# Kernel tuning notes

Hardware: AMD Instinct MI355X
Metric: run time of the kernel (lower is better)

Reference implementation:

```python
import jax, jax.numpy as jnp
import numpy as np

D_MODEL = 1024
N_HEAD = 16
HEAD_DIM = D_MODEL // N_HEAD
D_INNER = (int(D_MODEL * 2.0) + 7) // 8 * 8  # 2048
EPS = 1e-6


def setup_inputs() -> dict:
    key = jax.random.key(0)
    ks = jax.random.split(key, 8)
    B, T = 2, 2048
    s = 0.02
    return {
        "x": jax.random.normal(ks[0], (B, T, D_MODEL), dtype=jnp.float32),
        "ln1_w": jnp.ones((D_MODEL,), jnp.float32),
        "ln2_w": jnp.ones((D_MODEL,), jnp.float32),
        "qkv_w": jax.random.normal(ks[1], (3 * D_MODEL, D_MODEL), jnp.float32) * s,
        "o_w": jax.random.normal(ks[2], (D_MODEL, D_MODEL), jnp.float32) * s,
        "gate_w": jax.random.normal(ks[3], (D_INNER, D_MODEL), jnp.float32) * s,
        "up_w": jax.random.normal(ks[4], (D_INNER, D_MODEL), jnp.float32) * s,
        "down_w": jax.random.normal(ks[5], (D_MODEL, D_INNER), jnp.float32) * s,
    }


def _rmsnorm(x, w):
    xf = x.astype(jnp.float32)
    rms = jax.lax.rsqrt(jnp.mean(xf * xf, axis=-1, keepdims=True) + EPS)
    return (xf * rms).astype(x.dtype) * w


def _attention(x, qkv_w, o_w):
    B, T, D = x.shape
    qkv = (x @ qkv_w.T).reshape(B, T, 3, N_HEAD, HEAD_DIM)
    q, k, v = qkv[:, :, 0], qkv[:, :, 1], qkv[:, :, 2]  # [B,T,H,hd]
    scale = 1.0 / np.sqrt(HEAD_DIM)
    att = jnp.einsum("bqhd,bkhd->bhqk", q, k) * scale
    causal = jnp.tril(jnp.ones((T, T), dtype=bool))
    att = jnp.where(causal[None, None], att, -jnp.inf)
    att = jax.nn.softmax(att, axis=-1)
    y = jnp.einsum("bhqk,bkhd->bqhd", att, v).reshape(B, T, D)
    return y @ o_w.T


def _ffn(x, gate_w, up_w, down_w):
    g = jax.nn.silu(x @ gate_w.T)
    u = x @ up_w.T
    return (g * u) @ down_w.T


def reference(x, ln1_w, ln2_w, qkv_w, o_w, gate_w, up_w, down_w):
    x = x + _attention(_rmsnorm(x, ln1_w), qkv_w, o_w)
    x = x + _ffn(_rmsnorm(x, ln2_w), gate_w, up_w, down_w)
    return x
```

## Files before the change

kernel.cpp:

```cpp
#include <hip/hip_runtime.h>
#include <hip/hip_bf16.h>
#include <cstdint>

typedef __hip_bfloat16 bf16;
typedef __attribute__((ext_vector_type(8))) short bf16x8;
typedef __attribute__((ext_vector_type(4))) float f32x4;
typedef __attribute__((ext_vector_type(4))) int i32x4;

#define T_SEQ 2048
#define DMODEL 1024
#define NHEAD 16
#define DHEAD 64
#define MROWS 4096

typedef const __attribute__((address_space(1))) void* gas_ptr;
typedef __attribute__((address_space(3))) void* las_ptr;

static __device__ __forceinline__ f32x4 mfma16(bf16x8 a, bf16x8 b, f32x4 c) {
  return __builtin_amdgcn_mfma_f32_16x16x32_bf16(a, b, c, 0, 0, 0);
}
static __device__ __forceinline__ void gload_lds16(const void* g, void* l) {
  __builtin_amdgcn_global_load_lds((gas_ptr)g, (las_ptr)l, 16, 0, 0);
}
static __device__ __forceinline__ float b2f(unsigned short u) {
  union { unsigned int i; float f; } x; x.i = ((unsigned int)u) << 16; return x.f;
}
static __device__ __forceinline__ unsigned short f2bu(float f) {
  __hip_bfloat16 h = __float2bfloat16(f);
  unsigned short u; __builtin_memcpy(&u, &h, 2); return u;
}

__global__ __launch_bounds__(256) void f2ball_k(const float* __restrict__ a,
                                                const float* __restrict__ b,
                                                const float* __restrict__ c,
                                                const float* __restrict__ d,
                                                const float* __restrict__ e,
                                                bf16* __restrict__ out) {
  const int idx = (blockIdx.x * 256 + threadIdx.x) * 4;
  const float* src;
  int off, dst;
  if (idx < 3145728) {
    src = a; off = idx; dst = idx;
  } else if (idx < 4194304) {
    src = b; off = idx - 3145728; dst = idx;
  } else if (idx < 6291456) {
    src = c; off = idx - 4194304;
    dst = 4194304 + ((off >> 10) << 11) + (off & 1023);
  } else if (idx < 8388608) {
    src = d; off = idx - 6291456;
    dst = 4194304 + ((off >> 10) << 11) + 1024 + (off & 1023);
  } else {
    src = e; off = idx - 8388608; dst = idx;
  }
  const float4 v = *(const float4*)(src + off);
  ushort4 ov;
  ov.x = f2bu(v.x); ov.y = f2bu(v.y); ov.z = f2bu(v.z); ov.w = f2bu(v.w);
  *(ushort4*)((unsigned short*)out + dst) = ov;
}

__global__ __launch_bounds__(256) void rms_k(const float* __restrict__ x,
                                             const float* __restrict__ w,
                                             bf16* __restrict__ out) {
  const int row = blockIdx.x;
  const int tid = threadIdx.x;
  const float4 v = ((const float4*)(x + (size_t)row * DMODEL))[tid];
  float ss = v.x * v.x + v.y * v.y + v.z * v.z + v.w * v.w;
#pragma unroll
  for (int off = 32; off; off >>= 1) ss += __shfl_xor(ss, off);
  __shared__ float red[4];
  if ((tid & 63) == 0) red[tid >> 6] = ss;
  __syncthreads();
  const float tot = red[0] + red[1] + red[2] + red[3];
  const float rinv = rsqrtf(tot * (1.f / DMODEL) + 1e-6f);
  const float4 wv = ((const float4*)w)[tid];
  bf16* o = out + (size_t)row * DMODEL + tid * 4;
  o[0] = __float2bfloat16(v.x * rinv * wv.x);
  o[1] = __float2bfloat16(v.y * rinv * wv.y);
  o[2] = __float2bfloat16(v.z * rinv * wv.z);
  o[3] = __float2bfloat16(v.w * rinv * wv.w);
}

template <int K, int EPI>
__global__ __launch_bounds__(256) void gemm_bt(const bf16* __restrict__ A,
                                               const bf16* __restrict__ Bw, int N,
                                               void* __restrict__ o0, void* __restrict__ o1,
                                               void* __restrict__ o2,
                                               const float* __restrict__ res) {
  __shared__ bf16 As[128 * 32];
  __shared__ bf16 Bs[128 * 32];
  const int bn0 = blockIdx.x * 128;
  const int bm0 = blockIdx.y * 128;
  const int tid = threadIdx.x;
  const int wave = tid >> 6, lane = tid & 63;
  const int wr = wave >> 1, wc = wave & 1;
  const int fr = lane & 15, g8 = (lane >> 4) * 8, r4 = (lane >> 4) * 4;
  const int srow = lane >> 2;
  const int scol = (lane & 3) * 8;

  const f32x4 fzero = {0.f, 0.f, 0.f, 0.f};
  f32x4 acc[4][4];
#pragma unroll
  for (int i = 0; i < 4; i++)
#pragma unroll
    for (int j = 0; j < 4; j++) acc[i][j] = fzero;

  const bf16* gA0 = A + (size_t)(bm0 + wave * 16 + srow) * K + scol;
  const bf16* gA1 = A + (size_t)(bm0 + (wave + 4) * 16 + srow) * K + scol;
  const bf16* gB0 = Bw + (size_t)(bn0 + wave * 16 + srow) * K + scol;
  const bf16* gB1 = Bw + (size_t)(bn0 + (wave + 4) * 16 + srow) * K + scol;

  for (int k0 = 0; k0 < K; k0 += 32) {
    gload_lds16(gA0 + k0, &As[wave * 512]);
    gload_lds16(gA1 + k0, &As[(wave + 4) * 512]);
    gload_lds16(gB0 + k0, &Bs[wave * 512]);
    gload_lds16(gB1 + k0, &Bs[(wave + 4) * 512]);
    __syncthreads();
    bf16x8 af[4], bfr[4];
#pragma unroll
    for (int mr = 0; mr < 4; mr++)
      af[mr] = *(const bf16x8*)&As[(wr * 64 + mr * 16 + fr) * 32 + g8];
#pragma unroll
    for (int nr = 0; nr < 4; nr++)
      bfr[nr] = *(const bf16x8*)&Bs[(wc * 64 + nr * 16 + fr) * 32 + g8];
#pragma unroll
    for (int mr = 0; mr < 4; mr++)
#pragma unroll
      for (int nr = 0; nr < 4; nr++)
        acc[mr][nr] = mfma16(af[mr], bfr[nr], acc[mr][nr]);
    __syncthreads();
  }

#pragma unroll
  for (int mr = 0; mr < 4; mr++) {
#pragma unroll
    for (int nr = 0; nr < 4; nr++) {
#pragma unroll
      for (int r = 0; r < 4; r++) {
        const int row = bm0 + wr * 64 + mr * 16 + r4 + r;
        const int col = bn0 + wc * 64 + nr * 16 + fr;
        const float vsum = acc[mr][nr][r];
        if (EPI == 0) {
          ((bf16*)o0)[(size_t)row * N + col] = __float2bfloat16(vsum);
        } else if (EPI == 1) {
          const int sel = col >> 10;
          const int n = col & 1023;
          const int h = n >> 6, d = n & 63;
          const int b = row >> 11, t = row & 2047;
          if (sel == 2) {
            ((bf16*)o2)[(((size_t)(b * NHEAD + h)) * DHEAD + d) * T_SEQ + t] =
                __float2bfloat16(vsum);
          } else {
            bf16* dst = (sel == 0) ? (bf16*)o0 : (bf16*)o1;
            dst[(((size_t)(b * NHEAD + h)) * T_SEQ + t) * DHEAD + d] = __float2bfloat16(vsum);
          }
        } else if (EPI == 2) {
          ((float*)o0)[(size_t)row * N + col] = res[(size_t)row * N + col] + vsum;
        } else {
          const float other = __shfl_xor(vsum, 1);
          if ((fr & 1) == 0) {
            const float g = vsum, u = other;
            const float s = g / (1.f + __expf(-g));
            ((bf16*)o0)[(size_t)row * (N >> 1) + (col >> 1)] =
                __float2bfloat16(s * u);
          }
        }
      }
    }
  }
}

__global__ __launch_bounds__(256) void attn_k(const bf16* __restrict__ qb,
                                              const bf16* __restrict__ kb,
                                              const bf16* __restrict__ vt,
                                              bf16* __restrict__ y,
                                              unsigned short* __restrict__ pO,
                                              float* __restrict__ pL) {
  const int wave = threadIdx.x >> 6, lane = threadIdx.x & 63;
  const int bid = blockIdx.x;
  int bh, qt, ks0, nb, heavy, hs;
  if (bid < 1024) {
    const int c = bid & 7, r = bid >> 3;
    bh = c * 4 + (r & 3);
    const int idx = r >> 2;
    qt = 31 - (idx >> 1);
    hs = idx & 1;
    heavy = 1;
    nb = qt + 1;
    ks0 = hs * nb;
  } else {
    const int bd = bid - 1024;
    const int c = bd & 7, r = bd >> 3;
    bh = c * 4 + (r & 3);
    qt = 15 - (r >> 2);
    hs = 0;
    heavy = 0;
    nb = 2 * qt + 2;
    ks0 = 0;
  }
  const int b = bh >> 4, h = bh & 15;
  const int fr = lane & 15, g8 = (lane >> 4) * 8, r4 = (lane >> 4) * 4;
  const int u = lane >> 4;
  const int src1 = fr + ((u & 1) << 5);
  const int src2 = src1 + 16;
  const bool hB = u >= 2;

  const bf16* qp = qb + (size_t)bh * T_SEQ * DHEAD;
  const bf16* kp = kb + (size_t)bh * T_SEQ * DHEAD;
  const bf16* vp = vt + (size_t)bh * DHEAD * T_SEQ;

  __shared__ char Ks[2][4096];
  __shared__ char Vs[2][4096];

  const int q0 = qt * 64 + wave * 16;
  const int kend = q0 + 16;
  const int qrow = q0 + fr;

  const bf16x8 qf0 = *(const bf16x8*)(qp + (size_t)(q0 + fr) * DHEAD + g8);
  const bf16x8 qf1 = *(const bf16x8*)(qp + (size_t)(q0 + fr) * DHEAD + 32 + g8);

  const int krow_l = lane >> 3;
  const int kslot_l = (lane & 7) ^ krow_l;
  const int vrow_l = lane >> 2;
  const int vslot_l = (lane & 3) ^ ((lane >> 3) & 3);

  const int kswz = (fr & 7) << 4;
  const int koffA = fr * 128 + ((u * 16) ^ kswz);
  const int koffB = fr * 128 + (((4 + u) * 16) ^ kswz);
  const int vswz = ((fr >> 1) & 3) << 4;

  const f32x4 fzero = {0.f, 0.f, 0.f, 0.f};
  f32x4 acc[4];
  float lpart = 0.f;
#pragma unroll
  for (int nf = 0; nf < 4; nf++) acc[nf] = fzero;

  gload_lds16(kp + (size_t)(ks0 * 32 + wave * 8 + krow_l) * DHEAD + kslot_l * 8,
              &Ks[0][wave * 1024]);
  gload_lds16(vp + (size_t)(wave * 16 + vrow_l) * T_SEQ + ks0 * 32 + vslot_l * 8,
              &Vs[0][wave * 1024]);
  __syncthreads();

  for (int ts = 0; ts < nb; ++ts) {
    const int kt = (ks0 + ts) * 32;
    const int buf = ts & 1;
    if (ts + 1 < nb) {
      const int kn = kt + 32;
      gload_lds16(kp + (size_t)(kn + wave * 8 + krow_l) * DHEAD + kslot_l * 8,
                  &Ks[buf ^ 1][wave * 1024]);
      gload_lds16(vp + (size_t)(wave * 16 + vrow_l) * T_SEQ + kn + vslot_l * 8,
                  &Vs[buf ^ 1][wave * 1024]);
    }
    if (kt < kend) {
      const char* KB = Ks[buf];
      const char* VB = Vs[buf];
      const bf16x8 kf0a = *(const bf16x8*)(KB + koffA);
      const bf16x8 kf0b = *(const bf16x8*)(KB + koffB);
      const bf16x8 kf1a = *(const bf16x8*)(KB + 2048 + koffA);
      const bf16x8 kf1b = *(const bf16x8*)(KB + 2048 + koffB);
      bf16x8 vf[4];
#pragma unroll
      for (int nf = 0; nf < 4; nf++)
        vf[nf] = *(const bf16x8*)(VB + (nf * 16 + fr) * 64 + ((u * 16) ^ vswz));

      f32x4 s0 = mfma16(kf0a, qf0, fzero);
      s0 = mfma16(kf0b, qf1, s0);
      f32x4 s1 = mfma16(kf1a, qf0, fzero);
      s1 = mfma16(kf1b, qf1, s1);

      float x0[4], x1[4];
      if (kt + 31 < q0) {
#pragma unroll
        for (int r = 0; r < 4; r++) {
          x0[r] = __expf(fminf(s0[r] * 0.125f, 30.f));
          x1[r] = __expf(fminf(s1[r] * 0.125f, 30.f));
          lpart += x0[r] + x1[r];
        }
      } else {
#pragma unroll
        for (int r = 0; r < 4; r++) {
          const int k0 = kt + r4 + r;
          const int k1 = k0 + 16;
          x0[r] = (k0 <= qrow) ? __expf(fminf(s0[r] * 0.125f, 30.f)) : 0.f;
          x1[r] = (k1 <= qrow) ? __expf(fminf(s1[r] * 0.125f, 30.f)) : 0.f;
          lpart += x0[r] + x1[r];
        }
      }

      const int A01 = (int)((unsigned)f2bu(x0[0]) | ((unsigned)f2bu(x0[1]) << 16));
      const int A23 = (int)((unsigned)f2bu(x0[2]) | ((unsigned)f2bu(x0[3]) << 16));
      const int B01 = (int)((unsigned)f2bu(x1[0]) | ((unsigned)f2bu(x1[1]) << 16));
      const int B23 = (int)((unsigned)f2bu(x1[2]) | ((unsigned)f2bu(x1[3]) << 16));

      const int t0a = __shfl(A01, src1), t0b = __shfl(B01, src1);
      const int t1a = __shfl(A23, src1), t1b = __shfl(B23, src1);
      const int t2a = __shfl(A01, src2), t2b = __shfl(B01, src2);
      const int t3a = __shfl(A23, src2), t3b = __shfl(B23, src2);
      i32x4 pw;
      pw[0] = hB ? t0b : t0a;
      pw[1] = hB ? t1b : t1a;
      pw[2] = hB ? t2b : t2a;
      pw[3] = hB ? t3b : t3a;
      const bf16x8 pb = __builtin_bit_cast(bf16x8, pw);

#pragma unroll
      for (int nf = 0; nf < 4; nf++) acc[nf] = mfma16(vf[nf], pb, acc[nf]);
    }
    __syncthreads();
  }

  lpart += __shfl_xor(lpart, 16);
  lpart += __shfl_xor(lpart, 32);

  if (!heavy) {
    const float inv = 1.f / lpart;
    const int t = q0 + fr;
    unsigned short* yb =
        (unsigned short*)(y + (((size_t)(b * T_SEQ + t)) * NHEAD + h) * DHEAD);
#pragma unroll
    for (int nf = 0; nf < 4; nf++) {
      ushort4 ov;
      ov.x = f2bu(acc[nf][0] * inv);
      ov.y = f2bu(acc[nf][1] * inv);
      ov.z = f2bu(acc[nf][2] * inv);
      ov.w = f2bu(acc[nf][3] * inv);
      *(ushort4*)(yb + nf * 16 + r4) = ov;
    }
  } else {
    const int tl = q0 - 1024 + fr;
    unsigned short* po = pO + ((size_t)(hs * 32 + bh) * 1024 + tl) * DHEAD;
#pragma unroll
    for (int nf = 0; nf < 4; nf++) {
      ushort4 ov;
      ov.x = f2bu(acc[nf][0]);
      ov.y = f2bu(acc[nf][1]);
      ov.z = f2bu(acc[nf][2]);
      ov.w = f2bu(acc[nf][3]);
      *(ushort4*)(po + nf * 16 + r4) = ov;
    }
    if (lane < 16) pL[(size_t)(hs * 32 + bh) * 1024 + (q0 - 1024) + lane] = lpart;
  }
}

__global__ __launch_bounds__(256) void comb_k(const unsigned short* __restrict__ pO,
                                              const float* __restrict__ pL,
                                              bf16* __restrict__ y) {
  const int idx = blockIdx.x * 256 + threadIdx.x;
  const int row = idx >> 4;
  const int d0 = (idx & 15) * 4;
  const int bh = row >> 10, tl = row & 1023;
  const int b = bh >> 4, h = bh & 15;
  const int t = 1024 + tl;
  const float inv = 1.f / (pL[row] + pL[32768 + row]);
  const ushort4 a = *(const ushort4*)(pO + (size_t)row * DHEAD + d0);
  const ushort4 c = *(const ushort4*)(pO + (size_t)(32768 + row) * DHEAD + d0);
  ushort4 ov;
  ov.x = f2bu((b2f(a.x) + b2f(c.x)) * inv);
  ov.y = f2bu((b2f(a.y) + b2f(c.y)) * inv);
  ov.z = f2bu((b2f(a.z) + b2f(c.z)) * inv);
  ov.w = f2bu((b2f(a.w) + b2f(c.w)) * inv);
  *(ushort4*)((unsigned short*)y + (((size_t)(b * T_SEQ + t)) * NHEAD + h) * DHEAD + d0) = ov;
}

extern "C" void kernel_launch(void* const* d_in, const int* in_sizes, int n_in,
                              void* d_out, int out_size, void* d_ws, size_t ws_size,
                              hipStream_t stream) {
  const float* x     = (const float*)d_in[0];
  const float* ln1w  = (const float*)d_in[1];
  const float* ln2w  = (const float*)d_in[2];
  const float* qkvw  = (const float*)d_in[3];
  const float* ow    = (const float*)d_in[4];
  const float* gatew = (const float*)d_in[5];
  const float* upw   = (const float*)d_in[6];
  const float* downw = (const float*)d_in[7];

  uint8_t* ws = (uint8_t*)d_ws;
  bf16* WQKV = (bf16*)(ws + 0);
  bf16* WO   = (bf16*)(ws + 6291456);
  bf16* WGU  = (bf16*)(ws + 8388608);
  bf16* WD   = (bf16*)(ws + 16777216);
  bf16* H    = (bf16*)(ws + 20971520);
  bf16* Q    = (bf16*)(ws + 29360128);
  bf16* Kb   = (bf16*)(ws + 37748736);
  bf16* VT   = (bf16*)(ws + 46137344);
  bf16* Y    = (bf16*)(ws + 54525952);
  float* X2  = (float*)(ws + 62914560);
  bf16* G = (bf16*)(ws + 29360128);
  unsigned short* pO = (unsigned short*)(ws + 62914560);
  float* pL = (float*)(ws + 20971520);

  f2ball_k<<<10240, 256, 0, stream>>>(qkvw, ow, gatew, upw, downw, (bf16*)ws);

  rms_k<<<MROWS, 256, 0, stream>>>(x, ln1w, H);
  gemm_bt<1024, 1><<<dim3(24, 32), 256, 0, stream>>>(H, WQKV, 3072, Q, Kb, VT, nullptr);
  attn_k<<<1536, 256, 0, stream>>>(Q, Kb, VT, Y, pO, pL);
  comb_k<<<2048, 256, 0, stream>>>(pO, pL, Y);
  gemm_bt<1024, 2><<<dim3(8, 32), 256, 0, stream>>>(Y, WO, 1024, X2, nullptr, nullptr, x);

  rms_k<<<MROWS, 256, 0, stream>>>(X2, ln2w, H);
  gemm_bt<1024, 4><<<dim3(32, 32), 256, 0, stream>>>(H, WGU, 4096, G, nullptr, nullptr, nullptr);
  gemm_bt<2048, 2><<<dim3(8, 32), 256, 0, stream>>>(G, WD, 1024, (float*)d_out, nullptr, nullptr, X2);
}
```

Measured before the change: 237.6 us.

## Double-buffer GEMM LDS tiles with async global-to-LDS prefetch two stages ahead

The GEMM main loop now uses two LDS buffers for the A and B tiles. It issues the global_load_lds for tile t+2 right after computing tile t and waits on vmcnt(4) so the load of the next tile overlaps with MFMA work. The goal is to hide global memory latency that was previously fully exposed by the load-then-sync pattern. It doubles LDS use per block, which may reduce occupancy, and depends on hand-placed waitcnt and barrier instructions being correct.

```diff
diff --git a/kernel.cpp b/kernel.cpp
--- a/kernel.cpp
+++ b/kernel.cpp
@@ -86,8 +86,8 @@
                                                void* __restrict__ o0, void* __restrict__ o1,
                                                void* __restrict__ o2,
                                                const float* __restrict__ res) {
-  __shared__ bf16 As[128 * 32];
-  __shared__ bf16 Bs[128 * 32];
+  __shared__ bf16 As[2][128 * 32];
+  __shared__ bf16 Bs[2][128 * 32];
   const int bn0 = blockIdx.x * 128;
   const int bm0 = blockIdx.y * 128;
   const int tid = threadIdx.x;
@@ -109,25 +109,41 @@
   const bf16* gB0 = Bw + (size_t)(bn0 + wave * 16 + srow) * K + scol;
   const bf16* gB1 = Bw + (size_t)(bn0 + (wave + 4) * 16 + srow) * K + scol;
 
-  for (int k0 = 0; k0 < K; k0 += 32) {
-    gload_lds16(gA0 + k0, &As[wave * 512]);
-    gload_lds16(gA1 + k0, &As[(wave + 4) * 512]);
-    gload_lds16(gB0 + k0, &Bs[wave * 512]);
-    gload_lds16(gB1 + k0, &Bs[(wave + 4) * 512]);
-    __syncthreads();
+  auto stage = [&](int k0, int bufi) {
+    gload_lds16(gA0 + k0, &As[bufi][wave * 512]);
+    gload_lds16(gA1 + k0, &As[bufi][(wave + 4) * 512]);
+    gload_lds16(gB0 + k0, &Bs[bufi][wave * 512]);
+    gload_lds16(gB1 + k0, &Bs[bufi][(wave + 4) * 512]);
+  };
+
+  constexpr int NT = K / 32;
+  stage(0, 0);
+  stage(32, 1);
+
+  for (int t = 0; t < NT; ++t) {
+    if (t + 1 < NT)
+      asm volatile("s_waitcnt vmcnt(4)" ::: "memory");
+    else
+      asm volatile("s_waitcnt vmcnt(0)" ::: "memory");
+    __builtin_amdgcn_s_barrier();
+    asm volatile("" ::: "memory");
+    const int cb = t & 1;
     bf16x8 af[4], bfr[4];
 #pragma unroll
     for (int mr = 0; mr < 4; mr++)
-      af[mr] = *(const bf16x8*)&As[(wr * 64 + mr * 16 + fr) * 32 + g8];
+      af[mr] = *(const bf16x8*)&As[cb][(wr * 64 + mr * 16 + fr) * 32 + g8];
 #pragma unroll
     for (int nr = 0; nr < 4; nr++)
-      bfr[nr] = *(const bf16x8*)&Bs[(wc * 64 + nr * 16 + fr) * 32 + g8];
+      bfr[nr] = *(const bf16x8*)&Bs[cb][(wc * 64 + nr * 16 + fr) * 32 + g8];
 #pragma unroll
     for (int mr = 0; mr < 4; mr++)
 #pragma unroll
       for (int nr = 0; nr < 4; nr++)
         acc[mr][nr] = mfma16(af[mr], bfr[nr], acc[mr][nr]);
-    __syncthreads();
+    asm volatile("s_waitcnt lgkmcnt(0)" ::: "memory");
+    __builtin_amdgcn_s_barrier();
+    asm volatile("" ::: "memory");
+    if (t + 2 < NT) stage((t + 2) * 32, cb);
   }
 
 #pragma unroll
```

Result: slower. 261.1 us (+9.9%).

## Add 256x256 double-buffered GEMM kernel for QKV and gate/up projections

Applied to the files above, without the earlier changes.

Adds a new 512-thread GEMM with 256x256 output tiles, a K-step of 64, double-buffered LDS staging via direct global-to-LDS loads, and an XOR-swizzled LDS layout to avoid bank conflicts. It is used for the QKV projection and the fused gate/up projection, which are the two widest GEMMs. The older 128x128 kernel is reduced to the residual-add epilogue and kept for the output and down projections. Larger tiles give more data reuse per byte loaded and overlap loads with MFMA, but they cut the grid to 192 and 256 blocks, which may underfill the CUs on MI355X, and they use 128 KB of LDS per block.

```diff
diff --git a/kernel.cpp b/kernel.cpp
--- a/kernel.cpp
+++ b/kernel.cpp
@@ -80,11 +80,10 @@
   o[3] = __float2bfloat16(v.w * rinv * wv.w);
 }
 
-template <int K, int EPI>
+template <int K>
 __global__ __launch_bounds__(256) void gemm_bt(const bf16* __restrict__ A,
                                                const bf16* __restrict__ Bw, int N,
-                                               void* __restrict__ o0, void* __restrict__ o1,
-                                               void* __restrict__ o2,
+                                               float* __restrict__ o0,
                                                const float* __restrict__ res) {
   __shared__ bf16 As[128 * 32];
   __shared__ bf16 Bs[128 * 32];
@@ -138,10 +137,97 @@
       for (int r = 0; r < 4; r++) {
         const int row = bm0 + wr * 64 + mr * 16 + r4 + r;
         const int col = bn0 + wc * 64 + nr * 16 + fr;
+        o0[(size_t)row * N + col] = res[(size_t)row * N + col] + acc[mr][nr][r];
+      }
+    }
+  }
+}
+
+template <int K, int EPI>
+__global__ __launch_bounds__(512) void gemm256(const bf16* __restrict__ A,
+                                               const bf16* __restrict__ Bw, int N,
+                                               void* __restrict__ o0,
+                                               void* __restrict__ o1,
+                                               void* __restrict__ o2) {
+  __shared__ bf16 As[2][256 * 64];
+  __shared__ bf16 Bs[2][256 * 64];
+  const int bn0 = blockIdx.x * 256;
+  const int bm0 = blockIdx.y * 256;
+  const int tid = threadIdx.x;
+  const int wave = tid >> 6, lane = tid & 63;
+  const int wr = wave >> 2, wc = wave & 3;
+  const int fr = lane & 15, u = lane >> 4, r4 = u * 4;
+
+  const int srow = lane >> 3;
+  const int sslot = (lane & 7) ^ srow;
+
+  const f32x4 fzero = {0.f, 0.f, 0.f, 0.f};
+  f32x4 acc[8][4];
+#pragma unroll
+  for (int i = 0; i < 8; i++)
+#pragma unroll
+    for (int j = 0; j < 4; j++) acc[i][j] = fzero;
+
+  const bf16* gA = A + (size_t)(bm0 + wave * 8 + srow) * K + sslot * 8;
+  const bf16* gB = Bw + (size_t)(bn0 + wave * 8 + srow) * K + sslot * 8;
+
+  auto stage = [&](int k0, int bufi) {
+#pragma unroll
+    for (int i = 0; i < 4; i++)
+      gload_lds16(gA + (size_t)(i * 64) * K + k0, &As[bufi][(i * 64 + wave * 8) * 64]);
+#pragma unroll
+    for (int i = 0; i < 4; i++)
+      gload_lds16(gB + (size_t)(i * 64) * K + k0, &Bs[bufi][(i * 64 + wave * 8) * 64]);
+  };
+
+  constexpr int NT = K / 64;
+  stage(0, 0);
+  stage(64, 1);
+
+  const int arow = wr * 128 + fr;
+  const int brow = wc * 64 + fr;
+
+  for (int t = 0; t < NT; ++t) {
+    if (t + 1 < NT)
+      asm volatile("s_waitcnt vmcnt(8)" ::: "memory");
+    else
+      asm volatile("s_waitcnt vmcnt(0)" ::: "memory");
+    __builtin_amdgcn_s_barrier();
+    __builtin_amdgcn_sched_barrier(0);
+    const int cb = t & 1;
+    const bf16* AB = As[cb];
+    const bf16* BB = Bs[cb];
+#pragma unroll
+    for (int kh = 0; kh < 2; kh++) {
+      const int slot = ((kh * 4 + u) ^ (fr & 7)) * 8;
+      bf16x8 bfr[4];
+#pragma unroll
+      for (int nr = 0; nr < 4; nr++)
+        bfr[nr] = *(const bf16x8*)&BB[(brow + nr * 16) * 64 + slot];
+#pragma unroll
+      for (int mr = 0; mr < 8; mr++) {
+        const bf16x8 af = *(const bf16x8*)&AB[(arow + mr * 16) * 64 + slot];
+#pragma unroll
+        for (int nr = 0; nr < 4; nr++)
+          acc[mr][nr] = mfma16(af, bfr[nr], acc[mr][nr]);
+      }
+    }
+    asm volatile("s_waitcnt lgkmcnt(0)" ::: "memory");
+    __builtin_amdgcn_s_barrier();
+    __builtin_amdgcn_sched_barrier(0);
+    if (t + 2 < NT) stage((t + 2) * 64, cb);
+  }
+
+#pragma unroll
+  for (int mr = 0; mr < 8; mr++) {
+#pragma unroll
+    for (int nr = 0; nr < 4; nr++) {
+#pragma unroll
+      for (int r = 0; r < 4; r++) {
+        const int row = bm0 + wr * 128 + mr * 16 + r4 + r;
+        const int col = bn0 + wc * 64 + nr * 16 + fr;
         const float vsum = acc[mr][nr][r];
-        if (EPI == 0) {
-          ((bf16*)o0)[(size_t)row * N + col] = __float2bfloat16(vsum);
-        } else if (EPI == 1) {
+        if (EPI == 1) {
           const int sel = col >> 10;
           const int n = col & 1023;
           const int h = n >> 6, d = n & 63;
@@ -153,15 +239,12 @@
             bf16* dst = (sel == 0) ? (bf16*)o0 : (bf16*)o1;
             dst[(((size_t)(b * NHEAD + h)) * T_SEQ + t) * DHEAD + d] = __float2bfloat16(vsum);
           }
-        } else if (EPI == 2) {
-          ((float*)o0)[(size_t)row * N + col] = res[(size_t)row * N + col] + vsum;
         } else {
           const float other = __shfl_xor(vsum, 1);
           if ((fr & 1) == 0) {
-            const float g = vsum, u = other;
+            const float g = vsum, uu = other;
             const float s = g / (1.f + __expf(-g));
-            ((bf16*)o0)[(size_t)row * (N >> 1) + (col >> 1)] =
-                __float2bfloat16(s * u);
+            ((bf16*)o0)[(size_t)row * (N >> 1) + (col >> 1)] = __float2bfloat16(s * uu);
           }
         }
       }
@@ -391,12 +474,12 @@
   f2ball_k<<<10240, 256, 0, stream>>>(qkvw, ow, gatew, upw, downw, (bf16*)ws);
 
   rms_k<<<MROWS, 256, 0, stream>>>(x, ln1w, H);
-  gemm_bt<1024, 1><<<dim3(24, 32), 256, 0, stream>>>(H, WQKV, 3072, Q, Kb, VT, nullptr);
+  gemm256<1024, 1><<<dim3(12, 16), 512, 0, stream>>>(H, WQKV, 3072, Q, Kb, VT);
   attn_k<<<1536, 256, 0, stream>>>(Q, Kb, VT, Y, pO, pL);
   comb_k<<<2048, 256, 0, stream>>>(pO, pL, Y);
-  gemm_bt<1024, 2><<<dim3(8, 32), 256, 0, stream>>>(Y, WO, 1024, X2, nullptr, nullptr, x);
+  gemm_bt<1024><<<dim3(8, 32), 256, 0, stream>>>(Y, WO, 1024, X2, x);
 
   rms_k<<<MROWS, 256, 0, stream>>>(X2, ln2w, H);
-  gemm_bt<1024, 4><<<dim3(32, 32), 256, 0, stream>>>(H, WGU, 4096, G, nullptr, nullptr, nullptr);
-  gemm_bt<2048, 2><<<dim3(8, 32), 256, 0, stream>>>(G, WD, 1024, (float*)d_out, nullptr, nullptr, X2);
-}
+  gemm256<1024, 4><<<dim3(16, 16), 512, 0, stream>>>(H, WGU, 4096, G, nullptr, nullptr);
+  gemm_bt<2048><<<dim3(8, 32), 256, 0, stream>>>(G, WD, 1024, (float*)d_out, X2);
+}
```

After: 248.0 us. 4.4% more time.

## Double GEMM K-tile to 64 with XOR-swizzled LDS layout

Applied to the files above, without the earlier changes.

The GEMM mainloop now stages 64-wide K tiles instead of 32, which halves the number of barrier pairs per K sweep and gives each sync twice as many MFMAs. The LDS layout uses an XOR swizzle on 16-byte slots so fragment reads avoid bank conflicts with the wider 128-byte rows. LDS use per block doubles to 32KB, which may reduce occupancy. There is still no double buffering, so loads are not overlapped with compute.

```diff
diff --git a/kernel.cpp b/kernel.cpp
--- a/kernel.cpp
+++ b/kernel.cpp
@@ -86,16 +86,17 @@
                                                void* __restrict__ o0, void* __restrict__ o1,
                                                void* __restrict__ o2,
                                                const float* __restrict__ res) {
-  __shared__ bf16 As[128 * 32];
-  __shared__ bf16 Bs[128 * 32];
+  __shared__ bf16 As[128 * 64];
+  __shared__ bf16 Bs[128 * 64];
   const int bn0 = blockIdx.x * 128;
   const int bm0 = blockIdx.y * 128;
   const int tid = threadIdx.x;
   const int wave = tid >> 6, lane = tid & 63;
   const int wr = wave >> 1, wc = wave & 1;
-  const int fr = lane & 15, g8 = (lane >> 4) * 8, r4 = (lane >> 4) * 4;
-  const int srow = lane >> 2;
-  const int scol = (lane & 3) * 8;
+  const int fr = lane & 15, u = lane >> 4, r4 = u * 4;
+  const int srow = lane >> 3;
+  const int sslot = (lane & 7) ^ srow;
+  const int fsw = fr & 7;
 
   const f32x4 fzero = {0.f, 0.f, 0.f, 0.f};
   f32x4 acc[4][4];
@@ -104,29 +105,33 @@
 #pragma unroll
     for (int j = 0; j < 4; j++) acc[i][j] = fzero;
 
-  const bf16* gA0 = A + (size_t)(bm0 + wave * 16 + srow) * K + scol;
-  const bf16* gA1 = A + (size_t)(bm0 + (wave + 4) * 16 + srow) * K + scol;
-  const bf16* gB0 = Bw + (size_t)(bn0 + wave * 16 + srow) * K + scol;
-  const bf16* gB1 = Bw + (size_t)(bn0 + (wave + 4) * 16 + srow) * K + scol;
-
-  for (int k0 = 0; k0 < K; k0 += 32) {
-    gload_lds16(gA0 + k0, &As[wave * 512]);
-    gload_lds16(gA1 + k0, &As[(wave + 4) * 512]);
-    gload_lds16(gB0 + k0, &Bs[wave * 512]);
-    gload_lds16(gB1 + k0, &Bs[(wave + 4) * 512]);
+  const bf16* gA = A + (size_t)(bm0 + wave * 32 + srow) * K + sslot * 8;
+  const bf16* gB = Bw + (size_t)(bn0 + wave * 32 + srow) * K + sslot * 8;
+
+  for (int k0 = 0; k0 < K; k0 += 64) {
+#pragma unroll
+    for (int j = 0; j < 4; j++)
+      gload_lds16(gA + (size_t)(j * 8) * K + k0, &As[(wave * 32 + j * 8) * 64]);
+#pragma unroll
+    for (int j = 0; j < 4; j++)
+      gload_lds16(gB + (size_t)(j * 8) * K + k0, &Bs[(wave * 32 + j * 8) * 64]);
     __syncthreads();
-    bf16x8 af[4], bfr[4];
-#pragma unroll
-    for (int mr = 0; mr < 4; mr++)
-      af[mr] = *(const bf16x8*)&As[(wr * 64 + mr * 16 + fr) * 32 + g8];
-#pragma unroll
-    for (int nr = 0; nr < 4; nr++)
-      bfr[nr] = *(const bf16x8*)&Bs[(wc * 64 + nr * 16 + fr) * 32 + g8];
-#pragma unroll
-    for (int mr = 0; mr < 4; mr++)
+#pragma unroll
+    for (int kh = 0; kh < 2; kh++) {
+      const int slot8 = ((kh * 4 + u) ^ fsw) * 8;
+      bf16x8 af[4], bfr[4];
+#pragma unroll
+      for (int mr = 0; mr < 4; mr++)
+        af[mr] = *(const bf16x8*)&As[(wr * 64 + mr * 16 + fr) * 64 + slot8];
 #pragma unroll
       for (int nr = 0; nr < 4; nr++)
-        acc[mr][nr] = mfma16(af[mr], bfr[nr], acc[mr][nr]);
+        bfr[nr] = *(const bf16x8*)&Bs[(wc * 64 + nr * 16 + fr) * 64 + slot8];
+#pragma unroll
+      for (int mr = 0; mr < 4; mr++)
+#pragma unroll
+        for (int nr = 0; nr < 4; nr++)
+          acc[mr][nr] = mfma16(af[mr], bfr[nr], acc[mr][nr]);
+    }
     __syncthreads();
   }
 
@@ -158,10 +163,10 @@
         } else {
           const float other = __shfl_xor(vsum, 1);
           if ((fr & 1) == 0) {
-            const float g = vsum, u = other;
+            const float g = vsum, uu = other;
             const float s = g / (1.f + __expf(-g));
             ((bf16*)o0)[(size_t)row * (N >> 1) + (col >> 1)] =
-                __float2bfloat16(s * u);
+                __float2bfloat16(s * uu);
           }
         }
       }
```

Measured after the change: 237.2 us. About the same (-0.2%).
